# Performance work log

Hardware: AMD Instinct MI355X
Metric: run time of the kernel (lower is better)

The kernel has to match this reference:

```python
import jax, jax.numpy as jnp
import numpy as np

B, S, DIM = 2, 2048, 2048
NH, NKV = 32, 8
HD = DIM // NH          # 64
NREP = NH // NKV        # 4
BASE = 10000.0


def setup_inputs() -> dict:
    key = jax.random.key(0)
    ks = jax.random.split(key, 5)
    x = jax.random.normal(ks[0], (B, S, DIM), dtype=jnp.float32)
    # causal mask, 1 = keep, 0 = masked (matches masked_fill(mask == 0, -inf))
    mask = jnp.tril(jnp.ones((S, S), dtype=jnp.float32))[None, None]
    scale = 0.02
    Wq = jax.random.normal(ks[1], (DIM, NH * HD), dtype=jnp.float32) * scale
    Wk = jax.random.normal(ks[2], (DIM, NKV * HD), dtype=jnp.float32) * scale
    Wv = jax.random.normal(ks[3], (DIM, NKV * HD), dtype=jnp.float32) * scale
    Wo = jax.random.normal(ks[4], (NH * HD, DIM), dtype=jnp.float32) * scale
    return {"x": x, "mask": mask, "Wq": Wq, "Wk": Wk, "Wv": Wv, "Wo": Wo}


def _rope_cos_sin(seq_len, head_dim, dtype):
    inv_freq = 1.0 / (BASE ** (jnp.arange(0, head_dim, 2, dtype=jnp.float32) / head_dim))
    t = jnp.arange(seq_len, dtype=jnp.float32)
    freqs = t[:, None] * inv_freq[None, :]            # [S, HD/2]
    return jnp.cos(freqs).astype(dtype), jnp.sin(freqs).astype(dtype)


def _apply_rope(x, cos, sin):
    # x: [B, H, S, HD]; cos/sin: [S, HD/2] broadcast over B,H
    x1, x2 = jnp.split(x, 2, axis=-1)
    c = cos[None, None]
    s = sin[None, None]
    return jnp.concatenate([x1 * c - x2 * s, x2 * c + x1 * s], axis=-1)


def reference(x, mask, Wq, Wk, Wv, Wo):
    b, s, _ = x.shape
    q = (x @ Wq).reshape(b, s, NH, HD).transpose(0, 2, 1, 3)   # [B,NH,S,HD]
    k = (x @ Wk).reshape(b, s, NKV, HD).transpose(0, 2, 1, 3)  # [B,NKV,S,HD]
    v = (x @ Wv).reshape(b, s, NKV, HD).transpose(0, 2, 1, 3)
    cos, sin = _rope_cos_sin(s, HD, x.dtype)
    q = _apply_rope(q, cos, sin)
    k = _apply_rope(k, cos, sin)
    # GQA: repeat kv heads
    k = jnp.repeat(k, NREP, axis=1)
    v = jnp.repeat(v, NREP, axis=1)
    scale = HD ** -0.5
    attn = jnp.einsum('bhqd,bhkd->bhqk', q, k) * scale
    attn = jnp.where(mask == 0, -jnp.inf, attn)
    attn = jax.nn.softmax(attn, axis=-1)
    out = jnp.einsum('bhqk,bhkd->bhqd', attn, v)
    out = out.transpose(0, 2, 1, 3).reshape(b, s, NH * HD)
    return out @ Wo
```

## Files before the change

### kernel.cpp

```cpp
#include <hip/hip_runtime.h>
#include <stdint.h>

typedef __attribute__((ext_vector_type(8))) short short8;
typedef __attribute__((ext_vector_type(4))) short short4v;
typedef __attribute__((ext_vector_type(4))) float float4v;
typedef __attribute__((ext_vector_type(16))) float f32x16;
typedef __attribute__((ext_vector_type(4))) int int4v;
typedef __attribute__((ext_vector_type(2))) int int2v;
typedef __attribute__((ext_vector_type(2))) unsigned int uint2v;

#define DEV __device__ __forceinline__

DEV ushort f2bf(float f){
  uint32_t u = __float_as_uint(f);
  u = (u + 0x7fffu + ((u >> 16) & 1u)) >> 16;
  return (ushort)u;
}
DEV float bf2f(ushort h){
  uint32_t u = ((uint32_t)h) << 16;
  return __uint_as_float(u);
}

DEV void gload16(const void* g, void* l){
  __builtin_amdgcn_global_load_lds((const __attribute__((address_space(1))) void*)g,
                                   (__attribute__((address_space(3))) void*)l, 16, 0, 0);
}

DEV uint32_t cvtpk(float lo, float hi){
  uint32_t d;
  asm("v_cvt_pk_bf16_f32 %0, %1, %2" : "=v"(d) : "v"(lo), "v"(hi));
  return d;
}

DEV uint2v plswap2(uint32_t a, uint32_t b){
  return __builtin_amdgcn_permlane32_swap(a, b, false, false);
}

__global__ __launch_bounds__(256) void k_prep(const float* __restrict__ x, const float* __restrict__ Wq,
                                              const float* __restrict__ Wk, const float* __restrict__ Wv,
                                              const float* __restrict__ Wo,
                                              ushort* __restrict__ xb, ushort* __restrict__ wqkvt,
                                              ushort* __restrict__ wot,
                                              float* __restrict__ cost, float* __restrict__ sint,
                                              float qscale){
  __shared__ float tile[32][33];
  const int bid = blockIdx.x;
  if (bid < 10240){
    const float* src; ushort* dst; int N, K, bx, by; float scale;
    if (bid < 4096){ src = Wq; dst = wqkvt; N = 2048; K = 2048; scale = qscale; bx = bid & 63; by = bid >> 6; }
    else if (bid < 5120){ int lb = bid - 4096; src = Wk; dst = wqkvt + (size_t)2048 * 2048; N = 512; K = 2048; scale = 1.f; bx = lb & 15; by = lb >> 4; }
    else if (bid < 6144){ int lb = bid - 5120; src = Wv; dst = wqkvt + (size_t)2560 * 2048; N = 512; K = 2048; scale = 1.f; bx = lb & 15; by = lb >> 4; }
    else { int lb = bid - 6144; src = Wo; dst = wot; N = 2048; K = 2048; scale = 1.f; bx = lb & 63; by = lb >> 6; }
    int c0 = bx * 32, r0 = by * 32;
    int tx = threadIdx.x & 31, ty = threadIdx.x >> 5;
    #pragma unroll
    for (int i = 0; i < 32; i += 8)
      tile[ty + i][tx] = src[(size_t)(r0 + ty + i) * N + (c0 + tx)];
    __syncthreads();
    #pragma unroll
    for (int i = 0; i < 32; i += 8)
      dst[(size_t)(c0 + ty + i) * K + (r0 + tx)] = f2bf(tile[tx][ty + i] * scale);
  } else if (bid < 10496){
    int i = (bid - 10240) * 256 + threadIdx.x;
    int s = i >> 5, d = i & 31;
    float inv = powf(10000.0f, -(float)d / 32.0f);
    float ang = (float)s * inv;
    float sv, cv;
    sincosf(ang, &sv, &cv);
    cost[i] = cv;
    sint[i] = sv;
  } else {
    int i = (bid - 10496) * 256 + threadIdx.x;
    float4v v = *(const float4v*)(x + (size_t)i * 4);
    short4v o;
    o[0] = (short)f2bf(v[0]); o[1] = (short)f2bf(v[1]);
    o[2] = (short)f2bf(v[2]); o[3] = (short)f2bf(v[3]);
    *(short4v*)(xb + (size_t)i * 4) = o;
  }
}

template<int BM, int BN, bool OUTF32, int MINW>
__global__ __launch_bounds__(512, MINW) void k_gemm8(const ushort* __restrict__ A, const ushort* __restrict__ Bt,
                                                     void* __restrict__ Cp, int M, int N, int K, int nbx){
  constexpr int WM = BM / 2, WN = BN / 4;
  constexpr int MR = WM / 16, NR = WN / 16, MP = MR / 4;
  constexpr int AISS = BM / 64, BISS = BN / 64, ISS = AISS + BISS;
  constexpr int BUFB = (BM + BN) * 128;
  __shared__ char lds[2 * BUFB];

  int wg = blockIdx.x;
  int cpx = (int)gridDim.x >> 3;
  wg = (wg & 7) * cpx + (wg >> 3);
  const int bn = wg % nbx, bm = wg / nbx;
  const int tid = threadIdx.x;
  const int w = tid >> 6, l = tid & 63, l15 = l & 15, hi = l >> 4;
  const int wr = w >> 2, wc = w & 3;

  const int r8 = tid >> 3;
  const int ce = ((tid & 7) ^ (r8 & 7)) << 3;
  const ushort* ag = A + (size_t)(bm * BM + r8) * K + ce;
  const ushort* bg = Bt + (size_t)(bn * BN + r8) * K + ce;

  float4v acc[MR][NR];
  #pragma unroll
  for (int a = 0; a < MR; ++a)
    #pragma unroll
    for (int b = 0; b < NR; ++b)
      acc[a][b] = (float4v){0.f, 0.f, 0.f, 0.f};

  auto stage = [&](int kt, int buf){
    char* ab = lds + buf * BUFB;
    char* bb = ab + BM * 128;
    #pragma unroll
    for (int i = 0; i < AISS; ++i)
      gload16(ag + (size_t)(i * 64) * K + kt * 64, ab + i * 8192 + tid * 16);
    #pragma unroll
    for (int i = 0; i < BISS; ++i)
      gload16(bg + (size_t)(i * 64) * K + kt * 64, bb + i * 8192 + tid * 16);
  };
  auto lda = [&](const char* ab, int mf, int kk)->short8{
    int row = wr * WM + mf * 16 + l15;
    int a = (row * 128 + kk * 64 + hi * 16) ^ ((row & 7) << 4);
    return *(const short8*)(ab + a);
  };
  auto ldb = [&](const char* bb, int nf, int kk)->short8{
    int row = wc * WN + nf * 16 + l15;
    int a = (row * 128 + kk * 64 + hi * 16) ^ ((row & 7) << 4);
    return *(const short8*)(bb + a);
  };

  const int nkt = K >> 6;
  stage(0, 0);
  for (int t = 0; t < nkt; ++t){
    if (t + 1 < nkt){
      stage(t + 1, (t + 1) & 1);
      if constexpr (ISS == 8)      asm volatile("s_waitcnt vmcnt(8)" ::: "memory");
      else if constexpr (ISS == 7) asm volatile("s_waitcnt vmcnt(7)" ::: "memory");
      else if constexpr (ISS == 6) asm volatile("s_waitcnt vmcnt(6)" ::: "memory");
      else                         asm volatile("s_waitcnt vmcnt(5)" ::: "memory");
    } else {
      asm volatile("s_waitcnt vmcnt(0)" ::: "memory");
    }
    __builtin_amdgcn_s_barrier();
    __builtin_amdgcn_sched_barrier(0);

    const char* ab = lds + (t & 1) * BUFB;
    const char* bb = ab + BM * 128;
    short8 bfr[NR][2];
    #pragma unroll
    for (int nf = 0; nf < NR; ++nf){ bfr[nf][0] = ldb(bb, nf, 0); bfr[nf][1] = ldb(bb, nf, 1); }
    short8 af[MP][2];
    #pragma unroll
    for (int ml = 0; ml < MP; ++ml){ af[ml][0] = lda(ab, ml, 0); af[ml][1] = lda(ab, ml, 1); }

    #pragma unroll
    for (int p = 0; p < 4; ++p){
      __builtin_amdgcn_s_barrier();
      asm volatile("s_waitcnt lgkmcnt(0)" ::: "memory");
      __builtin_amdgcn_sched_barrier(0);
      __builtin_amdgcn_s_setprio(1);
      #pragma unroll
      for (int ml = 0; ml < MP; ++ml)
        #pragma unroll
        for (int nf = 0; nf < NR; ++nf){
          const int mf = p * MP + ml;
          acc[mf][nf] = __builtin_amdgcn_mfma_f32_16x16x32_bf16(af[ml][0], bfr[nf][0], acc[mf][nf], 0, 0, 0);
          acc[mf][nf] = __builtin_amdgcn_mfma_f32_16x16x32_bf16(af[ml][1], bfr[nf][1], acc[mf][nf], 0, 0, 0);
        }
      __builtin_amdgcn_s_setprio(0);
      __builtin_amdgcn_sched_barrier(0);
      if (p < 3){
        #pragma unroll
        for (int ml = 0; ml < MP; ++ml){
          af[ml][0] = lda(ab, (p + 1) * MP + ml, 0);
          af[ml][1] = lda(ab, (p + 1) * MP + ml, 1);
        }
      }
      __builtin_amdgcn_s_barrier();
    }
  }

  #pragma unroll
  for (int mf = 0; mf < MR; ++mf){
    int row0 = bm * BM + wr * WM + mf * 16 + hi * 4;
    #pragma unroll
    for (int nf = 0; nf < NR; ++nf){
      int col = bn * BN + wc * WN + nf * 16 + l15;
      #pragma unroll
      for (int reg = 0; reg < 4; ++reg){
        size_t idx = (size_t)(row0 + reg) * N + col;
        if constexpr (OUTF32) ((float*)Cp)[idx] = acc[mf][nf][reg];
        else                  ((ushort*)Cp)[idx] = f2bf(acc[mf][nf][reg]);
      }
    }
  }
}

__global__ __launch_bounds__(256) void k_rope_vt(ushort* __restrict__ qkv, const float* __restrict__ cost,
                                                 const float* __restrict__ sint, ushort* __restrict__ vt){
  __shared__ ushort tile[64][72];
  const int bid = blockIdx.x;
  if (bid < 5120){
    int t = bid * 256 + threadIdx.x;
    int row = t / 320;
    int rem = t - row * 320;
    int head = rem >> 3, d0 = (rem & 7) * 4;
    int s = row & 2047;
    ushort* p = qkv + (size_t)row * 3072 + head * 64 + d0;
    short4v a = *(short4v*)p;
    short4v b = *(short4v*)(p + 32);
    float4v c  = *(const float4v*)(cost + s * 32 + d0);
    float4v sn = *(const float4v*)(sint + s * 32 + d0);
    short4v na, nb;
    #pragma unroll
    for (int j = 0; j < 4; ++j){
      float x1 = bf2f((ushort)a[j]), x2 = bf2f((ushort)b[j]);
      na[j] = (short)f2bf(x1 * c[j] - x2 * sn[j]);
      nb[j] = (short)f2bf(x2 * c[j] + x1 * sn[j]);
    }
    *(short4v*)p = na;
    *(short4v*)(p + 32) = nb;
  } else {
    int lb = bid - 5120;
    int g = lb >> 5, st = lb & 31;
    int b = g >> 3, hk = g & 7;
    const ushort* src = qkv + (size_t)(b * 2048 + st * 64) * 3072 + 2560 + hk * 64;
    int tid = threadIdx.x;
    #pragma unroll
    for (int i = 0; i < 2; ++i){
      int r = i * 32 + (tid >> 3), c8 = (tid & 7) * 8;
      short8 v = *(const short8*)(src + (size_t)r * 3072 + c8);
      #pragma unroll
      for (int j = 0; j < 8; ++j) tile[r][c8 + j] = (ushort)v[j];
    }
    __syncthreads();
    ushort* dst = vt + (size_t)g * 64 * 2048 + st * 64;
    #pragma unroll
    for (int i = 0; i < 2; ++i){
      int d = i * 32 + (tid >> 3), s8 = (tid & 7) * 8;
      short8 ov;
      #pragma unroll
      for (int j = 0; j < 8; ++j) ov[j] = (short)tile[s8 + j][d];
      *(short8*)(dst + (size_t)d * 2048 + s8) = ov;
    }
  }
}

__global__ __launch_bounds__(256) void k_attn7(const ushort* __restrict__ qkv, const ushort* __restrict__ vt,
                                               ushort* __restrict__ att){
  __shared__ __align__(16) char lds[2][16384];
  const int raw = blockIdx.x;
  const int xcd = raw & 7, slot = raw >> 3;
  const int qb = 15 - (slot >> 3);
  const int rem = slot & 7;
  const int gidx = xcd * 2 + (rem >> 2);
  const int b = gidx >> 3, hk = gidx & 7;
  const int h = hk * 4 + (rem & 3);
  const int tid = threadIdx.x;
  const int w = tid >> 6, l = tid & 63, ql = l & 31, g = l >> 5;
  const int qw = qb * 128 + w * 32;
  const int diag_t = (qw + 31) >> 6;
  const int swz = (ql & 7) << 4;

  short8 qf[4];
  {
    const ushort* qbase = qkv + (size_t)(b * 2048 + qw + ql) * 3072 + h * 64 + g * 8;
    #pragma unroll
    for (int ds = 0; ds < 4; ++ds) qf[ds] = *(const short8*)(qbase + ds * 16);
  }

  f32x16 o0, o1;
  #pragma unroll
  for (int r = 0; r < 16; ++r){ o0[r] = 0.f; o1[r] = 0.f; }
  float l_part = 0.f;

  const int srow = tid >> 3;
  const int ce = ((tid & 7) ^ (srow & 7)) << 3;
  const ushort* kg = qkv + (size_t)(b * 2048 + srow) * 3072 + 2048 + hk * 64 + ce;
  const ushort* vg = vt + (size_t)gidx * 64 * 2048 + (size_t)srow * 2048 + ce;
  const int nt = qb * 2 + 2;

  auto stage = [&](int t, int buf){
    char* lb = lds[buf];
    #pragma unroll
    for (int i = 0; i < 2; ++i)
      gload16(kg + (size_t)(t * 64 + i * 32) * 3072, lb + i * 4096 + tid * 16);
    #pragma unroll
    for (int i = 0; i < 2; ++i)
      gload16(vg + (size_t)(i * 32) * 2048 + t * 64, lb + 8192 + i * 4096 + tid * 16);
  };

  stage(0, 0);
  for (int t = 0; t < nt; ++t){
    asm volatile("s_waitcnt vmcnt(0)" ::: "memory");
    __builtin_amdgcn_s_barrier();
    __builtin_amdgcn_sched_barrier(0);
    if (t + 1 < nt) stage(t + 1, (t + 1) & 1);

    if (t <= diag_t){
      const char* Kb = lds[t & 1];
      const char* Vb = Kb + 8192;

      f32x16 sa0, sa1;
      #pragma unroll
      for (int r = 0; r < 16; ++r){ sa0[r] = 0.f; sa1[r] = 0.f; }
      __builtin_amdgcn_s_setprio(1);
      #pragma unroll
      for (int ds = 0; ds < 4; ++ds){
        int cb = (ds * 32 + g * 16) ^ swz;
        short8 k0 = *(const short8*)(Kb + ql * 128 + cb);
        short8 k1 = *(const short8*)(Kb + (32 + ql) * 128 + cb);
        sa0 = __builtin_amdgcn_mfma_f32_32x32x16_bf16(k0, qf[ds], sa0, 0, 0, 0);
        sa1 = __builtin_amdgcn_mfma_f32_32x32x16_bf16(k1, qf[ds], sa1, 0, 0, 0);
      }
      __builtin_amdgcn_s_setprio(0);

      if (t == diag_t){
        int thr = qw + ql - t * 64;
        #pragma unroll
        for (int r = 0; r < 16; ++r){
          int kl = (r & 3) + 8 * (r >> 2) + 4 * g;
          sa0[r] = (kl > thr) ? -3e38f : sa0[r];
          sa1[r] = (kl + 32 > thr) ? -3e38f : sa1[r];
        }
      }

      uint32_t wds[2][8];
      float ps0 = 0.f, ps1 = 0.f, ps2 = 0.f, ps3 = 0.f;
      #pragma unroll
      for (int r = 0; r < 16; ++r){
        float p0 = __builtin_amdgcn_exp2f(sa0[r]);
        float p1 = __builtin_amdgcn_exp2f(sa1[r]);
        sa0[r] = p0; sa1[r] = p1;
        if ((r & 1) == 0){ ps0 += p0; ps1 += p1; }
        else { ps2 += p0; ps3 += p1; }
      }
      l_part += (ps0 + ps2) + (ps1 + ps3);
      #pragma unroll
      for (int u = 0; u < 8; ++u){
        wds[0][u] = cvtpk(sa0[2 * u], sa0[2 * u + 1]);
        wds[1][u] = cvtpk(sa1[2 * u], sa1[2 * u + 1]);
      }

      __builtin_amdgcn_s_setprio(1);
      #pragma unroll
      for (int ks = 0; ks < 4; ++ks){
        const int s2 = ks >> 1, c4 = (ks & 1) * 4;
        uint2v e0 = plswap2(wds[s2][c4 + 0], wds[s2][c4 + 2]);
        uint2v e1 = plswap2(wds[s2][c4 + 1], wds[s2][c4 + 3]);
        union { int4v w4; short8 s8; } pb;
        pb.w4[0] = (int)e0[0]; pb.w4[1] = (int)e1[0];
        pb.w4[2] = (int)e0[1]; pb.w4[3] = (int)e1[1];
        int cb = (ks * 32 + g * 16) ^ swz;
        short8 v0 = *(const short8*)(Vb + ql * 128 + cb);
        short8 v1 = *(const short8*)(Vb + (32 + ql) * 128 + cb);
        o0 = __builtin_amdgcn_mfma_f32_32x32x16_bf16(v0, pb.s8, o0, 0, 0, 0);
        o1 = __builtin_amdgcn_mfma_f32_32x32x16_bf16(v1, pb.s8, o1, 0, 0, 0);
      }
      __builtin_amdgcn_s_setprio(0);
    }
  }

  float lf;
  {
    uint2v lm = plswap2(__float_as_uint(l_part), __float_as_uint(l_part));
    lf = __uint_as_float(lm[0]) + __uint_as_float(lm[1]);
  }
  float invl = 1.0f / lf;
  ushort* ob = att + (size_t)(b * 2048 + qw + ql) * 2048 + h * 64;
  #pragma unroll
  for (int dm = 0; dm < 2; ++dm){
    #pragma unroll
    for (int rg = 0; rg < 4; ++rg){
      float f0 = (dm ? o1[4 * rg + 0] : o0[4 * rg + 0]) * invl;
      float f1 = (dm ? o1[4 * rg + 1] : o0[4 * rg + 1]) * invl;
      float f2 = (dm ? o1[4 * rg + 2] : o0[4 * rg + 2]) * invl;
      float f3 = (dm ? o1[4 * rg + 3] : o0[4 * rg + 3]) * invl;
      int2v wv;
      wv[0] = (int)cvtpk(f0, f1);
      wv[1] = (int)cvtpk(f2, f3);
      int d0 = dm * 32 + 8 * rg + 4 * g;
      *(int2v*)(ob + d0) = wv;
    }
  }
}

extern "C" void kernel_launch(void* const* d_in, const int* in_sizes, int n_in,
                              void* d_out, int out_size, void* d_ws, size_t ws_size,
                              hipStream_t stream) {
  const float* x  = (const float*)d_in[0];
  const float* Wq = (const float*)d_in[2];
  const float* Wk = (const float*)d_in[3];
  const float* Wv = (const float*)d_in[4];
  const float* Wo = (const float*)d_in[5];

  char* ws = (char*)d_ws;
  ushort* xb    = (ushort*)(ws);
  ushort* wqkvt = (ushort*)(ws + (16u << 20));
  ushort* wot   = (ushort*)(ws + (28u << 20));
  ushort* qkv   = (ushort*)(ws + (36u << 20));
  ushort* att   = (ushort*)(ws + (60u << 20));
  ushort* vt    = (ushort*)(ws + (76u << 20));
  float*  cost  = (float*)(ws + (80u << 20));
  float*  sint  = (float*)(ws + (80u << 20) + 262144);

  const float qscale = 0.125f * 1.4426950408889634f;

  k_prep<<<18688, 256, 0, stream>>>(x, Wq, Wk, Wv, Wo, xb, wqkvt, wot, cost, sint, qscale);
  k_gemm8<128, 192, false, 4><<<512, 512, 0, stream>>>(xb, wqkvt, qkv, 4096, 3072, 2048, 16);
  k_rope_vt<<<5632, 256, 0, stream>>>(qkv, cost, sint, vt);
  k_attn7<<<1024, 256, 0, stream>>>(qkv, vt, att);
  k_gemm8<128, 256, true, 2><<<256, 512, 0, stream>>>(att, wot, d_out, 4096, 2048, 2048, 8);
}
```

Baseline: 175.3 us.

## Restructure GEMM prefetch sync, MFMA row-sum in attention, smaller output GEMM tiles

The GEMM main loop now waits for all outstanding global loads and then issues the next tile's prefetch after the barrier. It also drops the per-phase barriers inside the K-step, cutting synchronisation while still overlapping loads with MFMA work. The attention kernel computes the softmax denominator with an extra MFMA against a ones vector instead of VALU accumulation and a cross-lane swap, trading VALU work for more matrix-core issue. The output projection switches from 128x256 to 128x128 tiles on 512 workgroups with higher occupancy, to improve CU fill.

```diff
diff --git a/kernel.cpp b/kernel.cpp
--- a/kernel.cpp
+++ b/kernel.cpp
@@ -84,7 +84,7 @@
                                                      void* __restrict__ Cp, int M, int N, int K, int nbx){
   constexpr int WM = BM / 2, WN = BN / 4;
   constexpr int MR = WM / 16, NR = WN / 16, MP = MR / 4;
-  constexpr int AISS = BM / 64, BISS = BN / 64, ISS = AISS + BISS;
+  constexpr int AISS = BM / 64, BISS = BN / 64;
   constexpr int BUFB = (BM + BN) * 128;
   __shared__ char lds[2 * BUFB];
 
@@ -132,17 +132,10 @@
   const int nkt = K >> 6;
   stage(0, 0);
   for (int t = 0; t < nkt; ++t){
-    if (t + 1 < nkt){
-      stage(t + 1, (t + 1) & 1);
-      if constexpr (ISS == 8)      asm volatile("s_waitcnt vmcnt(8)" ::: "memory");
-      else if constexpr (ISS == 7) asm volatile("s_waitcnt vmcnt(7)" ::: "memory");
-      else if constexpr (ISS == 6) asm volatile("s_waitcnt vmcnt(6)" ::: "memory");
-      else                         asm volatile("s_waitcnt vmcnt(5)" ::: "memory");
-    } else {
-      asm volatile("s_waitcnt vmcnt(0)" ::: "memory");
-    }
+    asm volatile("s_waitcnt vmcnt(0)" ::: "memory");
     __builtin_amdgcn_s_barrier();
     __builtin_amdgcn_sched_barrier(0);
+    if (t + 1 < nkt) stage(t + 1, (t + 1) & 1);
 
     const char* ab = lds + (t & 1) * BUFB;
     const char* bb = ab + BM * 128;
@@ -155,7 +148,6 @@
 
     #pragma unroll
     for (int p = 0; p < 4; ++p){
-      __builtin_amdgcn_s_barrier();
       asm volatile("s_waitcnt lgkmcnt(0)" ::: "memory");
       __builtin_amdgcn_sched_barrier(0);
       __builtin_amdgcn_s_setprio(1);
@@ -176,7 +168,6 @@
           af[ml][1] = lda(ab, (p + 1) * MP + ml, 1);
         }
       }
-      __builtin_amdgcn_s_barrier();
     }
   }
 
@@ -246,7 +237,7 @@
   }
 }
 
-__global__ __launch_bounds__(256) void k_attn7(const ushort* __restrict__ qkv, const ushort* __restrict__ vt,
+__global__ __launch_bounds__(256) void k_attn8(const ushort* __restrict__ qkv, const ushort* __restrict__ vt,
                                                ushort* __restrict__ att){
   __shared__ __align__(16) char lds[2][16384];
   const int raw = blockIdx.x;
@@ -268,11 +259,13 @@
     #pragma unroll
     for (int ds = 0; ds < 4; ++ds) qf[ds] = *(const short8*)(qbase + ds * 16);
   }
-
-  f32x16 o0, o1;
-  #pragma unroll
-  for (int r = 0; r < 16; ++r){ o0[r] = 0.f; o1[r] = 0.f; }
-  float l_part = 0.f;
+  short8 onesf;
+  #pragma unroll
+  for (int i = 0; i < 8; ++i) onesf[i] = (short)0x3F80;
+
+  f32x16 o0, o1, ladd;
+  #pragma unroll
+  for (int r = 0; r < 16; ++r){ o0[r] = 0.f; o1[r] = 0.f; ladd[r] = 0.f; }
 
   const int srow = tid >> 3;
   const int ce = ((tid & 7) ^ (srow & 7)) << 3;
@@ -326,20 +319,14 @@
       }
 
       uint32_t wds[2][8];
-      float ps0 = 0.f, ps1 = 0.f, ps2 = 0.f, ps3 = 0.f;
-      #pragma unroll
-      for (int r = 0; r < 16; ++r){
-        float p0 = __builtin_amdgcn_exp2f(sa0[r]);
-        float p1 = __builtin_amdgcn_exp2f(sa1[r]);
-        sa0[r] = p0; sa1[r] = p1;
-        if ((r & 1) == 0){ ps0 += p0; ps1 += p1; }
-        else { ps2 += p0; ps3 += p1; }
-      }
-      l_part += (ps0 + ps2) + (ps1 + ps3);
       #pragma unroll
       for (int u = 0; u < 8; ++u){
-        wds[0][u] = cvtpk(sa0[2 * u], sa0[2 * u + 1]);
-        wds[1][u] = cvtpk(sa1[2 * u], sa1[2 * u + 1]);
+        float a0 = __builtin_amdgcn_exp2f(sa0[2 * u]);
+        float a1 = __builtin_amdgcn_exp2f(sa0[2 * u + 1]);
+        wds[0][u] = cvtpk(a0, a1);
+        float b0 = __builtin_amdgcn_exp2f(sa1[2 * u]);
+        float b1 = __builtin_amdgcn_exp2f(sa1[2 * u + 1]);
+        wds[1][u] = cvtpk(b0, b1);
       }
 
       __builtin_amdgcn_s_setprio(1);
@@ -356,17 +343,13 @@
         short8 v1 = *(const short8*)(Vb + (32 + ql) * 128 + cb);
         o0 = __builtin_amdgcn_mfma_f32_32x32x16_bf16(v0, pb.s8, o0, 0, 0, 0);
         o1 = __builtin_amdgcn_mfma_f32_32x32x16_bf16(v1, pb.s8, o1, 0, 0, 0);
+        ladd = __builtin_amdgcn_mfma_f32_32x32x16_bf16(onesf, pb.s8, ladd, 0, 0, 0);
       }
       __builtin_amdgcn_s_setprio(0);
     }
   }
 
-  float lf;
-  {
-    uint2v lm = plswap2(__float_as_uint(l_part), __float_as_uint(l_part));
-    lf = __uint_as_float(lm[0]) + __uint_as_float(lm[1]);
-  }
-  float invl = 1.0f / lf;
+  float invl = 1.0f / ladd[0];
   ushort* ob = att + (size_t)(b * 2048 + qw + ql) * 2048 + h * 64;
   #pragma unroll
   for (int dm = 0; dm < 2; ++dm){
@@ -409,6 +392,6 @@
   k_prep<<<18688, 256, 0, stream>>>(x, Wq, Wk, Wv, Wo, xb, wqkvt, wot, cost, sint, qscale);
   k_gemm8<128, 192, false, 4><<<512, 512, 0, stream>>>(xb, wqkvt, qkv, 4096, 3072, 2048, 16);
   k_rope_vt<<<5632, 256, 0, stream>>>(qkv, cost, sint, vt);
-  k_attn7<<<1024, 256, 0, stream>>>(qkv, vt, att);
-  k_gemm8<128, 256, true, 2><<<256, 512, 0, stream>>>(att, wot, d_out, 4096, 2048, 2048, 8);
-}
+  k_attn8<<<1024, 256, 0, stream>>>(qkv, vt, att);
+  k_gemm8<128, 128, true, 4><<<512, 512, 0, stream>>>(att, wot, d_out, 4096, 2048, 2048, 16);
+}
```

Result: faster. 167.7 us (-4.4%).
